# Kernel tuning notes

Measured on AMD Instinct MI355X. Metric: run time of the kernel, lower is better.

The kernel has to match this reference:

```python
import jax, jax.numpy as jnp
import numpy as np

B, S, D, H, DH = 4, 2048, 1024, 16, 64
INIT_STD = 0.02
IGNORE = -100000.0


def setup_inputs() -> dict:
    key = jax.random.key(0)
    ks = jax.random.split(key, 5)
    x = jax.random.normal(ks[0], (B, S, D), dtype=jnp.float32)
    W_Q = INIT_STD * jax.random.normal(ks[1], (H, D, DH), dtype=jnp.float32)
    W_K = INIT_STD * jax.random.normal(ks[2], (H, D, DH), dtype=jnp.float32)
    W_V = INIT_STD * jax.random.normal(ks[3], (H, D, DH), dtype=jnp.float32)
    W_O = INIT_STD * jax.random.normal(ks[4], (H, DH, D), dtype=jnp.float32)
    b_Q = jnp.zeros((H, DH), dtype=jnp.float32)
    b_K = jnp.zeros((H, DH), dtype=jnp.float32)
    b_V = jnp.zeros((H, DH), dtype=jnp.float32)
    b_O = jnp.zeros((D,), dtype=jnp.float32)
    return {"x": x, "W_Q": W_Q, "b_Q": b_Q, "W_K": W_K, "b_K": b_K,
            "W_V": W_V, "b_V": b_V, "W_O": W_O, "b_O": b_O}


def reference(x, W_Q, b_Q, W_K, b_K, W_V, b_V, W_O, b_O):
    # x: (B, S, D); projections -> (B, S, H, DH)
    Q = jnp.einsum('bqd,hde->bqhe', x, W_Q) + b_Q
    K = jnp.einsum('bkd,hde->bkhe', x, W_K) + b_K
    V = jnp.einsum('bkd,hde->bkhe', x, W_V) + b_V
    d_head = Q.shape[-1]
    # scores: (B, H, Sq, Sk)
    scores = jnp.einsum('bqhe,bkhe->bhqk', Q, K) / np.sqrt(d_head).astype(np.float32)
    s = scores.shape[-1]
    causal = jnp.triu(jnp.ones((s, s), dtype=bool), k=1)
    scores = jnp.where(causal, jnp.float32(IGNORE), scores)
    A = jax.nn.softmax(scores, axis=-1)
    z = jnp.einsum('bhqk,bkhe->bqhe', A, V)
    # output projection: sum over heads + bias
    attn_out = jnp.einsum('bqhe,hed->bqd', z, W_O) + b_O
    return attn_out
```

## Files before the change

### kernel.cpp

```cpp
#include <hip/hip_runtime.h>


#define B_ 4
#define S_ 2048
#define D_ 1024
#define H_ 16
#define DH_ 64

typedef unsigned short ushort_t;
typedef __attribute__((ext_vector_type(4))) short short4v;
typedef __attribute__((ext_vector_type(8))) short short8v;
typedef __attribute__((ext_vector_type(4))) float floatx4;
typedef __attribute__((ext_vector_type(4))) unsigned short ushort4v;

static __device__ __forceinline__ ushort_t f2bf(float f) {
    union { float f; unsigned u; } v; v.f = f;
    unsigned r = v.u + 0x7fffu + ((v.u >> 16) & 1u);
    return (ushort_t)(r >> 16);
}

static __device__ __forceinline__ float fast_exp2(float x) {
#if __has_builtin(__builtin_amdgcn_exp2f)
    return __builtin_amdgcn_exp2f(x);
#else
    return exp2f(x);
#endif
}

static __device__ __forceinline__ unsigned pack_bf16_tr(float lo, float hi) {
    union { float f; unsigned u; } a, b;
    a.f = lo; b.f = hi;
    return __builtin_amdgcn_perm(b.u, a.u, 0x07060302u);
}

static __device__ __forceinline__ void g2lds16(const void* g, void* l) {
    __builtin_amdgcn_global_load_lds(
        (__attribute__((address_space(1))) void*)(unsigned long long)(size_t)g,
        (__attribute__((address_space(3))) void*)(unsigned int)(size_t)l,
        16, 0, 0);
}

__global__ void prep_kernel(const float* __restrict__ x,
                            const float* __restrict__ wq, const float* __restrict__ wk,
                            const float* __restrict__ wv, const float* __restrict__ wo,
                            ushort_t* __restrict__ xb, ushort_t* __restrict__ wt,
                            ushort_t* __restrict__ wot) {
    __shared__ float tile[32][33];
    int bid = blockIdx.x;
    int tid = threadIdx.x;
    if (bid < 8192) {
        int i = (bid * 256 + tid) * 4;
        float4 v = *(const float4*)&x[i];
        ushort4v o;
        o[0] = f2bf(v.x); o[1] = f2bf(v.y); o[2] = f2bf(v.z); o[3] = f2bf(v.w);
        *(ushort4v*)&xb[i] = o;
        return;
    }
    const float* src;
    ushort_t* d;
    int C, r0, c0;
    if (bid < 11264) {
        int t = bid - 8192;
        int z = t / 64, r = t % 64;
        src = (z < 16 ? wq : (z < 32 ? wk : wv)) + (size_t)(z & 15) * 65536;
        d = wt + (size_t)z * 65536;
        C = 64; r0 = (r >> 1) * 32; c0 = (r & 1) * 32;
    } else {
        int t = bid - 11264;
        int z = t / 64, r = t % 64;
        src = wo + (size_t)z * 65536;
        d = wot + (size_t)z * 64;
        C = 1024; r0 = (r & 1) * 32; c0 = (r >> 1) * 32;
    }
    int tx = tid & 31, ty = tid >> 5;
#pragma unroll
    for (int i = 0; i < 4; ++i)
        tile[ty + i * 8][tx] = src[(size_t)(r0 + ty + i * 8) * C + c0 + tx];
    __syncthreads();
#pragma unroll
    for (int i = 0; i < 4; ++i)
        d[(size_t)(c0 + ty + i * 8) * 1024 + r0 + tx] = f2bf(tile[tx][ty + i * 8]);
}

__global__ __launch_bounds__(256) void gemm_qkv(const ushort_t* __restrict__ A,
                                                const ushort_t* __restrict__ Wt,
                                                const float* __restrict__ bq,
                                                const float* __restrict__ bk,
                                                const float* __restrict__ bv,
                                                ushort_t* __restrict__ Qw,
                                                ushort_t* __restrict__ Kw,
                                                ushort_t* __restrict__ Vw) {
    __shared__ ushort_t sA[128 * 64];
    __shared__ ushort_t sB[128 * 64];
    const int tid = threadIdx.x;
    const int lane = tid & 63, w = tid >> 6;
    const int lq = lane & 15, quad = lane >> 4;
    const int wm = w >> 1, wn = w & 1;
    const int m0 = blockIdx.x * 128, n0 = blockIdx.y * 128;
    const int mat = blockIdx.y >> 3;

    floatx4 acc[4][4] = {};

    for (int k0 = 0; k0 < 1024; k0 += 64) {
        __syncthreads();
#pragma unroll
        for (int p = 0; p < 4; ++p) {
            int rr = w * 32 + p * 8 + (lane >> 3);
            int cc = (lane & 7) ^ (rr & 7);
            g2lds16(&A[(size_t)(m0 + rr) * 1024 + k0 + cc * 8], &sA[(w * 32 + p * 8) * 64]);
            g2lds16(&Wt[(size_t)(n0 + rr) * 1024 + k0 + cc * 8], &sB[(w * 32 + p * 8) * 64]);
        }
        __syncthreads();
#pragma unroll
        for (int ks = 0; ks < 2; ++ks) {
            short8v af[4], bfr[4];
#pragma unroll
            for (int t = 0; t < 4; ++t) {
                int ma = wm * 64 + t * 16 + lq;
                af[t] = *(const short8v*)&sA[ma * 64 + ((((ks << 2) | quad) ^ (ma & 7)) << 3)];
                int nb = wn * 64 + t * 16 + lq;
                bfr[t] = *(const short8v*)&sB[nb * 64 + ((((ks << 2) | quad) ^ (nb & 7)) << 3)];
            }
#pragma unroll
            for (int mt = 0; mt < 4; ++mt)
#pragma unroll
                for (int nt = 0; nt < 4; ++nt)
                    acc[mt][nt] = __builtin_amdgcn_mfma_f32_16x16x32_bf16(af[mt], bfr[nt], acc[mt][nt], 0, 0, 0);
        }
    }

    const float* bias = mat == 0 ? bq : (mat == 1 ? bk : bv);
    float bias_v[4];
#pragma unroll
    for (int nt = 0; nt < 4; ++nt) bias_v[nt] = bias[(n0 & 1023) + wn * 64 + nt * 16 + lq];

#pragma unroll
    for (int mt = 0; mt < 4; ++mt) {
#pragma unroll
        for (int nt = 0; nt < 4; ++nt) {
            int row0 = m0 + wm * 64 + mt * 16 + quad * 4;
            int col = (n0 & 1023) + wn * 64 + nt * 16 + lq;
            int h = col >> 6, e = col & 63;
            if (mat == 2) {
                int b = row0 >> 11, s = row0 & 2047;
                ushort4v pk;
#pragma unroll
                for (int rg = 0; rg < 4; ++rg) pk[rg] = f2bf(acc[mt][nt][rg] + bias_v[nt]);
                *(ushort4v*)&Vw[((size_t)((b << 4) | h) * 64 + e) * 2048 + s] = pk;
            } else {
                ushort_t* Du = mat == 0 ? Qw : Kw;
#pragma unroll
                for (int rg = 0; rg < 4; ++rg) {
                    int row = row0 + rg;
                    int b = row >> 11, s = row & 2047;
                    float v = acc[mt][nt][rg] + bias_v[nt];
                    if (mat == 0) v *= 0.18033688011112042f;
                    Du[((size_t)((b << 4) | h) * 2048 + s) * 64 + e] = f2bf(v);
                }
            }
        }
    }
}

#define VROW 140
__global__ __launch_bounds__(256) void attn_kernel(const ushort_t* __restrict__ Q,
                                                   const ushort_t* __restrict__ Kg,
                                                   const ushort_t* __restrict__ Vt,
                                                   ushort_t* __restrict__ Z) {
    __shared__ ushort_t sK[2][128 * 64];
    __shared__ ushort_t sV[64 * VROW];
    const int tid = threadIdx.x;
    const int lane = tid & 63, w = tid >> 6;
    const int lq = lane & 15, quad = lane >> 4;
    const int bh = blockIdx.x;
    const int b = bh >> 4, h = bh & 15;
    const ushort_t* Qp = Q + (size_t)bh * S_ * DH_;
    const ushort_t* Kp = Kg + (size_t)bh * S_ * DH_;
    const ushort_t* Vp = Vt + (size_t)bh * DH_ * S_;

    const int kbase0 = lq * 64 + ((quad ^ (lq & 7)) << 3);
    const int kbase1 = lq * 64 + (((4 | quad) ^ (lq & 7)) << 3);
    const int vbase = lq * VROW + quad * 4;
    const int vr = w * 16 + (lane >> 2);
    const int vc = (lane & 3) * 32;

    const floatx4 fzero = {0.f, 0.f, 0.f, 0.f};

    auto stageK = [&](int kt, int bs) __attribute__((always_inline)) {
        ushort_t* dK = sK[bs];
#pragma unroll
        for (int p = 0; p < 4; ++p) {
            int rrk = w * 32 + p * 8 + (lane >> 3);
            int ck = (lane & 7) ^ (rrk & 7);
            g2lds16(&Kp[(size_t)(kt * 128 + rrk) * 64 + ck * 8], &dK[(w * 32 + p * 8) * 64]);
        }
    };
    auto loadV = [&](int kt, short8v* vr4) __attribute__((always_inline)) {
        const ushort_t* src = &Vp[(size_t)vr * 2048 + kt * 128 + vc];
#pragma unroll
        for (int j = 0; j < 4; ++j) vr4[j] = *(const short8v*)&src[j * 8];
    };
    auto writeV = [&](const short8v* vr4) __attribute__((always_inline)) {
        ushort_t* dst = &sV[vr * VROW + vc];
#pragma unroll
        for (int j = 0; j < 4; ++j) *(short8v*)&dst[j * 8] = vr4[j];
    };

    for (int pass = 0; pass < 2; ++pass) {
        const int qt = pass == 0 ? (int)blockIdx.y : 15 - (int)blockIdx.y;
        const int q0 = qt * 128;

        short8v qf[2][2];
#pragma unroll
        for (int qi = 0; qi < 2; ++qi)
#pragma unroll
            for (int ks = 0; ks < 2; ++ks)
                qf[qi][ks] = *(const short8v*)&Qp[(size_t)(q0 + w * 32 + qi * 16 + lq) * DH_ + ks * 32 + quad * 8];

        float l_i[2] = {0.f, 0.f};
        floatx4 o[2][4] = {};
        short8v vreg[4];

        stageK(0, 0);
        loadV(0, vreg);

        for (int kt = 0; kt <= qt; ++kt) {
            const bool diag = (kt == qt);
            const ushort_t* cK = sK[kt & 1];

            __syncthreads();
            writeV(vreg);
            if (kt < qt) {
                stageK(kt + 1, (kt + 1) & 1);
                loadV(kt + 1, vreg);
            }

            floatx4 st[8][2];
#pragma unroll
            for (int si = 0; si < 8; ++si) {
                short8v a0 = *(const short8v*)&cK[kbase0 + si * 1024];
                short8v a1 = *(const short8v*)&cK[kbase1 + si * 1024];
#pragma unroll
                for (int qi = 0; qi < 2; ++qi) {
                    st[si][qi] = __builtin_amdgcn_mfma_f32_16x16x32_bf16(a0, qf[qi][0], fzero, 0, 0, 0);
                    st[si][qi] = __builtin_amdgcn_mfma_f32_16x16x32_bf16(a1, qf[qi][1], st[si][qi], 0, 0, 0);
                }
            }

            short4v pf[8][2];
#pragma unroll
            for (int qi = 0; qi < 2; ++qi) {
                const int qg = q0 + w * 32 + qi * 16 + lq;
                float lsum = 0.f;
#pragma unroll
                for (int si = 0; si < 8; ++si) {
                    float p[4];
#pragma unroll
                    for (int rg = 0; rg < 4; ++rg) {
                        float v = st[si][qi][rg];
                        if (diag) {
                            int sg = kt * 128 + si * 16 + quad * 4 + rg;
                            if (sg > qg) v = -1e30f;
                        }
                        p[rg] = fast_exp2(v);
                        lsum += p[rg];
                    }
                    union { unsigned u[2]; short4v v4; } pk;
                    pk.u[0] = pack_bf16_tr(p[0], p[1]);
                    pk.u[1] = pack_bf16_tr(p[2], p[3]);
                    pf[si][qi] = pk.v4;
                }
                l_i[qi] += lsum;
            }

            __syncthreads();

#pragma unroll
            for (int ksp = 0; ksp < 8; ++ksp) {
#pragma unroll
                for (int et = 0; et < 4; ++et) {
                    short4v vf = *(const short4v*)&sV[vbase + et * (16 * VROW) + ksp * 16];
#pragma unroll
                    for (int qi = 0; qi < 2; ++qi)
                        o[qi][et] = __builtin_amdgcn_mfma_f32_16x16x16bf16_1k(pf[ksp][qi], vf, o[qi][et], 0, 0, 0);
                }
            }
        }

#pragma unroll
        for (int qi = 0; qi < 2; ++qi) {
            float lf = l_i[qi];
            lf += __shfl_xor(lf, 16);
            lf += __shfl_xor(lf, 32);
            float linv[4];
#pragma unroll
            for (int rg = 0; rg < 4; ++rg) linv[rg] = 1.0f / __shfl(lf, quad * 4 + rg);
#pragma unroll
            for (int et = 0; et < 4; ++et) {
#pragma unroll
                for (int rg = 0; rg < 4; ++rg) {
                    int qg = q0 + w * 32 + qi * 16 + quad * 4 + rg;
                    int e = et * 16 + lq;
                    Z[((size_t)(b * S_ + qg) * H_ + h) * DH_ + e] = f2bf(o[qi][et][rg] * linv[rg]);
                }
            }
        }
    }
}

__global__ __launch_bounds__(256) void gemm_o(const ushort_t* __restrict__ A,
                                              const ushort_t* __restrict__ Bt,
                                              const float* __restrict__ bias,
                                              float* __restrict__ Dst) {
    __shared__ ushort_t sA[128 * 64];
    __shared__ ushort_t sB[128 * 64];
    const int tid = threadIdx.x;
    const int lane = tid & 63, w = tid >> 6;
    const int lq = lane & 15, quad = lane >> 4;
    const int wm = w >> 1, wn = w & 1;
    const int m0 = blockIdx.x * 128, n0 = blockIdx.y * 128;

    floatx4 acc[4][4] = {};

    for (int k0 = 0; k0 < 1024; k0 += 64) {
        __syncthreads();
#pragma unroll
        for (int p = 0; p < 4; ++p) {
            int rr = w * 32 + p * 8 + (lane >> 3);
            int cc = (lane & 7) ^ (rr & 7);
            g2lds16(&A[(size_t)(m0 + rr) * 1024 + k0 + cc * 8], &sA[(w * 32 + p * 8) * 64]);
            g2lds16(&Bt[(size_t)(n0 + rr) * 1024 + k0 + cc * 8], &sB[(w * 32 + p * 8) * 64]);
        }
        __syncthreads();
#pragma unroll
        for (int ks = 0; ks < 2; ++ks) {
            short8v af[4], bfr[4];
#pragma unroll
            for (int t = 0; t < 4; ++t) {
                int ma = wm * 64 + t * 16 + lq;
                af[t] = *(const short8v*)&sA[ma * 64 + ((((ks << 2) | quad) ^ (ma & 7)) << 3)];
                int nb = wn * 64 + t * 16 + lq;
                bfr[t] = *(const short8v*)&sB[nb * 64 + ((((ks << 2) | quad) ^ (nb & 7)) << 3)];
            }
#pragma unroll
            for (int mt = 0; mt < 4; ++mt)
#pragma unroll
                for (int nt = 0; nt < 4; ++nt)
                    acc[mt][nt] = __builtin_amdgcn_mfma_f32_16x16x32_bf16(af[mt], bfr[nt], acc[mt][nt], 0, 0, 0);
        }
    }

    float bias_v[4];
#pragma unroll
    for (int nt = 0; nt < 4; ++nt) bias_v[nt] = bias[n0 + wn * 64 + nt * 16 + lq];

#pragma unroll
    for (int mt = 0; mt < 4; ++mt) {
#pragma unroll
        for (int nt = 0; nt < 4; ++nt) {
            int row0 = m0 + wm * 64 + mt * 16 + quad * 4;
            int col = n0 + wn * 64 + nt * 16 + lq;
#pragma unroll
            for (int rg = 0; rg < 4; ++rg)
                Dst[(size_t)(row0 + rg) * 1024 + col] = acc[mt][nt][rg] + bias_v[nt];
        }
    }
}

extern "C" void kernel_launch(void* const* d_in, const int* in_sizes, int n_in,
                              void* d_out, int out_size, void* d_ws, size_t ws_size,
                              hipStream_t stream) {
    const float* x  = (const float*)d_in[0];
    const float* wq = (const float*)d_in[1];
    const float* bq = (const float*)d_in[2];
    const float* wk = (const float*)d_in[3];
    const float* bk = (const float*)d_in[4];
    const float* wv = (const float*)d_in[5];
    const float* bv = (const float*)d_in[6];
    const float* wo = (const float*)d_in[7];
    const float* bo = (const float*)d_in[8];

    char* ws = (char*)d_ws;
    size_t off = 0;
    ushort_t* xb  = (ushort_t*)(ws + off); off += (size_t)8192 * 1024 * 2;
    ushort_t* wt  = (ushort_t*)(ws + off); off += (size_t)3 * 1024 * 1024 * 2;
    ushort_t* wot = (ushort_t*)(ws + off); off += (size_t)1024 * 1024 * 2;
    ushort_t* Qw  = (ushort_t*)(ws + off); off += (size_t)8192 * 1024 * 2;
    ushort_t* Kw  = (ushort_t*)(ws + off); off += (size_t)8192 * 1024 * 2;
    ushort_t* Vw  = (ushort_t*)(ws + off); off += (size_t)8192 * 1024 * 2;
    ushort_t* Zw  = (ushort_t*)(ws + off); off += (size_t)8192 * 1024 * 2;

    prep_kernel<<<12288, 256, 0, stream>>>(x, wq, wk, wv, wo, xb, wt, wot);
    gemm_qkv<<<dim3(64, 24), 256, 0, stream>>>(xb, wt, bq, bk, bv, Qw, Kw, Vw);
    attn_kernel<<<dim3(64, 8), 256, 0, stream>>>(Qw, Kw, Vw, Zw);
    gemm_o<<<dim3(64, 8), 256, 0, stream>>>(Zw, wot, bo, (float*)d_out);
}
```

Before: 254.1 us.

## Restructure QKV GEMM into 256x256 double-buffered tiles with interleaved async staging

The QKV projection GEMM moves from 128x128 tiles with 4 warps and a single LDS buffer to 256x256 tiles with 8 warps and double-buffered LDS. Global-to-LDS copies for the next K step are interleaved with the MFMA phases of the current step, using explicit vmcnt waits, barriers, sched_barriers and setprio. The intent is to hide load latency and raise arithmetic intensity per tile. In exchange it uses more LDS (128KB) and accumulator registers, and the grid shrinks to 384 blocks, which may underfill 256 CUs.

```diff
diff --git a/kernel.cpp b/kernel.cpp
--- a/kernel.cpp
+++ b/kernel.cpp
@@ -82,64 +82,119 @@
         d[(size_t)(c0 + ty + i * 8) * 1024 + r0 + tx] = f2bf(tile[tx][ty + i * 8]);
 }
 
-__global__ __launch_bounds__(256) void gemm_qkv(const ushort_t* __restrict__ A,
-                                                const ushort_t* __restrict__ Wt,
-                                                const float* __restrict__ bq,
-                                                const float* __restrict__ bk,
-                                                const float* __restrict__ bv,
-                                                ushort_t* __restrict__ Qw,
-                                                ushort_t* __restrict__ Kw,
-                                                ushort_t* __restrict__ Vw) {
-    __shared__ ushort_t sA[128 * 64];
-    __shared__ ushort_t sB[128 * 64];
+
+#define GQ_BAR() __builtin_amdgcn_s_barrier()
+#define GQ_VM4 do { asm volatile("s_waitcnt vmcnt(4)"); __builtin_amdgcn_sched_barrier(0); } while (0)
+#define GQ_VM2 do { asm volatile("s_waitcnt vmcnt(2)"); __builtin_amdgcn_sched_barrier(0); } while (0)
+#define GQ_VM0 do { asm volatile("s_waitcnt vmcnt(0)"); __builtin_amdgcn_sched_barrier(0); } while (0)
+#define GQ_WAITLG do { asm volatile("s_waitcnt lgkmcnt(0)"); __builtin_amdgcn_sched_barrier(0); } while (0)
+
+#define GQ_READS_B(KB)                                                          \
+    _Pragma("unroll") for (int nt = 0; nt < 4; ++nt)                            \
+        bfr[KB][nt] = *(const short8v*)&cB[(wn * 64 + nt * 16) * 64 + ((KB) ? kb1 : kb0)];
+
+#define GQ_READS_A(MH, KB)                                                      \
+    _Pragma("unroll") for (int i = 0; i < 4; ++i)                               \
+        af[i] = *(const short8v*)&cA[(wm * 128 + ((MH) * 4 + i) * 16) * 64 + ((KB) ? kb1 : kb0)];
+
+#define GQ_MFMA(MH, KB)                                                         \
+    GQ_WAITLG;                                                                  \
+    __builtin_amdgcn_s_setprio(1);                                              \
+    _Pragma("unroll") for (int i = 0; i < 4; ++i)                               \
+        _Pragma("unroll") for (int nt = 0; nt < 4; ++nt)                        \
+            acc[(MH) * 4 + i][nt] = __builtin_amdgcn_mfma_f32_16x16x32_bf16(    \
+                af[i], bfr[KB][nt], acc[(MH) * 4 + i][nt], 0, 0, 0);            \
+    __builtin_amdgcn_s_setprio(0);                                              \
+    __builtin_amdgcn_sched_barrier(0);
+
+#define GQ_KSTEP(CA, CB, S1, S2, S3, S4, WMID, WEND) do {                       \
+    const ushort_t* cA = (CA); const ushort_t* cB = (CB);                       \
+    short8v af[4]; short8v bfr[2][4];                                           \
+    GQ_READS_B(0) GQ_READS_A(0, 0) S1; GQ_BAR();                                \
+    GQ_MFMA(0, 0) GQ_BAR();                                                     \
+    GQ_READS_B(1) GQ_READS_A(0, 1) S2; GQ_BAR();                                \
+    GQ_MFMA(0, 1) WMID; GQ_BAR();                                               \
+    GQ_READS_A(1, 0) S3; GQ_BAR();                                              \
+    GQ_MFMA(1, 0) GQ_BAR();                                                     \
+    GQ_READS_A(1, 1) S4; GQ_BAR();                                              \
+    GQ_MFMA(1, 1) WEND; GQ_BAR();                                               \
+} while (0)
+
+__global__ __launch_bounds__(512, 2) void gemm_qkv(const ushort_t* __restrict__ A,
+                                                   const ushort_t* __restrict__ Wt,
+                                                   const float* __restrict__ bq,
+                                                   const float* __restrict__ bk,
+                                                   const float* __restrict__ bv,
+                                                   ushort_t* __restrict__ Qw,
+                                                   ushort_t* __restrict__ Kw,
+                                                   ushort_t* __restrict__ Vw) {
+    __shared__ ushort_t sA[2][256 * 64];
+    __shared__ ushort_t sB[2][256 * 64];
     const int tid = threadIdx.x;
     const int lane = tid & 63, w = tid >> 6;
     const int lq = lane & 15, quad = lane >> 4;
-    const int wm = w >> 1, wn = w & 1;
-    const int m0 = blockIdx.x * 128, n0 = blockIdx.y * 128;
-    const int mat = blockIdx.y >> 3;
-
-    floatx4 acc[4][4] = {};
-
-    for (int k0 = 0; k0 < 1024; k0 += 64) {
-        __syncthreads();
-#pragma unroll
-        for (int p = 0; p < 4; ++p) {
-            int rr = w * 32 + p * 8 + (lane >> 3);
+    const int wm = w >> 2, wn = w & 3;
+    const int m0 = blockIdx.x * 256, n0 = blockIdx.y * 256;
+
+    const int kb0 = lq * 64 + ((quad ^ (lq & 7)) << 3);
+    const int kb1 = lq * 64 + (((4 | quad) ^ (lq & 7)) << 3);
+
+    const int uR = ((w & 4) << 5) + (w & 3) * 16;
+
+    auto stageA2 = [&](ushort_t* dst, int kk, int R0) __attribute__((always_inline)) {
+#pragma unroll
+        for (int j = 0; j < 2; ++j) {
+            int rr = R0 + j * 8 + (lane >> 3);
             int cc = (lane & 7) ^ (rr & 7);
-            g2lds16(&A[(size_t)(m0 + rr) * 1024 + k0 + cc * 8], &sA[(w * 32 + p * 8) * 64]);
-            g2lds16(&Wt[(size_t)(n0 + rr) * 1024 + k0 + cc * 8], &sB[(w * 32 + p * 8) * 64]);
-        }
-        __syncthreads();
-#pragma unroll
-        for (int ks = 0; ks < 2; ++ks) {
-            short8v af[4], bfr[4];
-#pragma unroll
-            for (int t = 0; t < 4; ++t) {
-                int ma = wm * 64 + t * 16 + lq;
-                af[t] = *(const short8v*)&sA[ma * 64 + ((((ks << 2) | quad) ^ (ma & 7)) << 3)];
-                int nb = wn * 64 + t * 16 + lq;
-                bfr[t] = *(const short8v*)&sB[nb * 64 + ((((ks << 2) | quad) ^ (nb & 7)) << 3)];
-            }
-#pragma unroll
-            for (int mt = 0; mt < 4; ++mt)
-#pragma unroll
-                for (int nt = 0; nt < 4; ++nt)
-                    acc[mt][nt] = __builtin_amdgcn_mfma_f32_16x16x32_bf16(af[mt], bfr[nt], acc[mt][nt], 0, 0, 0);
-        }
-    }
-
+            g2lds16(&A[(size_t)(m0 + rr) * 1024 + kk + cc * 8], &dst[(R0 + j * 8) * 64]);
+        }
+    };
+    auto stageB2 = [&](ushort_t* dst, int kk, int R0) __attribute__((always_inline)) {
+#pragma unroll
+        for (int j = 0; j < 2; ++j) {
+            int rr = R0 + j * 8 + (lane >> 3);
+            int cc = (lane & 7) ^ (rr & 7);
+            g2lds16(&Wt[(size_t)(n0 + rr) * 1024 + kk + cc * 8], &dst[(R0 + j * 8) * 64]);
+        }
+    };
+
+    floatx4 acc[8][4] = {};
+
+    stageA2(sA[0], 0, uR);
+    stageB2(sB[0], 0, w * 32);
+    stageB2(sB[0], 0, w * 32 + 16);
+    stageA2(sA[0], 0, uR + 64);
+    GQ_VM2;
+    GQ_BAR();
+
+    int p = 0;
+    for (int t = 0; t < 15; ++t) {
+        const int kk = (t + 1) * 64;
+        ushort_t* nA = sA[p ^ 1];
+        ushort_t* nB = sB[p ^ 1];
+        GQ_KSTEP(sA[p], sB[p],
+                 stageA2(nA, kk, uR),
+                 stageB2(nB, kk, w * 32),
+                 stageB2(nB, kk, w * 32 + 16),
+                 stageA2(nA, kk, uR + 64),
+                 GQ_VM4, GQ_VM2);
+        p ^= 1;
+    }
+    GQ_KSTEP(sA[1], sB[1], (void)0, (void)0, (void)0, (void)0, GQ_VM0, (void)0);
+
+    const int mat = blockIdx.y >> 2;
     const float* bias = mat == 0 ? bq : (mat == 1 ? bk : bv);
+    const int colbase = (blockIdx.y & 3) * 256 + wn * 64;
     float bias_v[4];
 #pragma unroll
-    for (int nt = 0; nt < 4; ++nt) bias_v[nt] = bias[(n0 & 1023) + wn * 64 + nt * 16 + lq];
-
-#pragma unroll
-    for (int mt = 0; mt < 4; ++mt) {
+    for (int nt = 0; nt < 4; ++nt) bias_v[nt] = bias[colbase + nt * 16 + lq];
+
+#pragma unroll
+    for (int mt = 0; mt < 8; ++mt) {
 #pragma unroll
         for (int nt = 0; nt < 4; ++nt) {
-            int row0 = m0 + wm * 64 + mt * 16 + quad * 4;
-            int col = (n0 & 1023) + wn * 64 + nt * 16 + lq;
+            int row0 = m0 + wm * 128 + mt * 16 + quad * 4;
+            int col = colbase + nt * 16 + lq;
             int h = col >> 6, e = col & 63;
             if (mat == 2) {
                 int b = row0 >> 11, s = row0 & 2047;
@@ -391,7 +446,7 @@
     ushort_t* Zw  = (ushort_t*)(ws + off); off += (size_t)8192 * 1024 * 2;
 
     prep_kernel<<<12288, 256, 0, stream>>>(x, wq, wk, wv, wo, xb, wt, wot);
-    gemm_qkv<<<dim3(64, 24), 256, 0, stream>>>(xb, wt, bq, bk, bv, Qw, Kw, Vw);
+    gemm_qkv<<<dim3(32, 12), 512, 0, stream>>>(xb, wt, bq, bk, bv, Qw, Kw, Vw);
     attn_kernel<<<dim3(64, 8), 256, 0, stream>>>(Qw, Kw, Vw, Zw);
     gemm_o<<<dim3(64, 8), 256, 0, stream>>>(Zw, wot, bo, (float*)d_out);
 }
```

Measured after the change: 254.8 us. About the same (+0.3%).
